# Performance work log

Measured on AMD Instinct MI355X. Metric: run time of the kernel, lower is better.

## Reference

```python
import jax, jax.numpy as jnp
import numpy as np

B, E, D = 4096, 64, 1024

def setup_inputs() -> dict:
    key = jax.random.key(0)
    k1, k2 = jax.random.split(key)
    z = jax.random.normal(k1, (B, D), dtype=jnp.float32)
    expert_keys = jax.random.normal(k2, (E, D), dtype=jnp.float32)
    log_sigma = jnp.zeros((D,), dtype=jnp.float32)
    return {"z": z, "expert_keys": expert_keys, "log_sigma": log_sigma}

def reference(z, expert_keys, log_sigma):
    # diag(sigma_inv) @ diff followed by (. * diff).sum(-1) is exactly an
    # elementwise-scaled squared distance: sum_d exp(-log_sigma_d) * diff_d^2
    sigma_inv = jnp.exp(-log_sigma)                              # [D]
    diff = z[:, None, :] - expert_keys[None, :, :]               # [B, E, D]
    mahalanobis_dist = jnp.einsum('bed,d,bed->be', diff, sigma_inv, diff)  # [B, E]
    similarity = 1.0 / (1.0 + mahalanobis_dist)                  # [B, E]
    weights = jax.nn.softmax(similarity, axis=-1)                # [B, E]
    weighted_expert = weights @ expert_keys                      # [B, D]
    return (similarity, weighted_expert)
```

## Files before the change

kernel.cpp:

```cpp
#include <hip/hip_runtime.h>
#include <hip/hip_bf16.h>

#define B_N 4096
#define E_N 64
#define D_N 1024

typedef __bf16 bf16x8 __attribute__((ext_vector_type(8)));
typedef __bf16 bf16x4 __attribute__((ext_vector_type(4)));
typedef float f32x4 __attribute__((ext_vector_type(4)));


__global__ __launch_bounds__(256) void prep_kernel(
    const float* __restrict__ keys, const float* __restrict__ lsig,
    float* __restrict__ sinv, float* __restrict__ ak,
    __bf16* __restrict__ sk, __bf16* __restrict__ kT)
{
  const int e = blockIdx.x;
  const int t = threadIdx.x;
  const float4 k4 = *(const float4*)(keys + e * D_N + 4 * t);
  const float4 l4 = *(const float4*)(lsig + 4 * t);
  float4 s4;
  s4.x = expf(-l4.x); s4.y = expf(-l4.y); s4.z = expf(-l4.z); s4.w = expf(-l4.w);
  if (e == 0) *(float4*)(sinv + 4 * t) = s4;
  const float4 sk4 = make_float4(s4.x * k4.x, s4.y * k4.y, s4.z * k4.z, s4.w * k4.w);
  bf16x4 skb;
  skb[0] = (__bf16)sk4.x; skb[1] = (__bf16)sk4.y; skb[2] = (__bf16)sk4.z; skb[3] = (__bf16)sk4.w;
  *(bf16x4*)(sk + e * D_N + 4 * t) = skb;
  kT[(4 * t + 0) * E_N + e] = (__bf16)k4.x;
  kT[(4 * t + 1) * E_N + e] = (__bf16)k4.y;
  kT[(4 * t + 2) * E_N + e] = (__bf16)k4.z;
  kT[(4 * t + 3) * E_N + e] = (__bf16)k4.w;
  float p = sk4.x * k4.x + sk4.y * k4.y + sk4.z * k4.z + sk4.w * k4.w;
  #pragma unroll
  for (int off = 32; off > 0; off >>= 1) p += __shfl_down(p, off);
  __shared__ float red[4];
  if ((t & 63) == 0) red[t >> 6] = p;
  __syncthreads();
  if (t == 0) ak[e] = red[0] + red[1] + red[2] + red[3];
}

__global__ __launch_bounds__(256) void main_kernel(
    const float* __restrict__ z, const float* __restrict__ sinv,
    const float* __restrict__ ak, const __bf16* __restrict__ sk,
    const __bf16* __restrict__ kT,
    float* __restrict__ out_sim, float* __restrict__ out_we)
{
  constexpr int ZS = D_N + 8;
  __shared__ __bf16 zlds[16 * ZS];
  __shared__ float azp[16][16];
  __shared__ float azs[16];
  __shared__ float simb[16][68];
  __shared__ __bf16 wlds[16][72];

  const int t  = threadIdx.x;
  const int b0 = blockIdx.x * 16;

  const int sr = t >> 4;
  const int sc = t & 15;
  const float* zrow = z + (size_t)(b0 + sr) * D_N;
  float azacc = 0.f;
  #pragma unroll
  for (int l = 0; l < 16; ++l) {
    const int c = sc * 4 + l * 64;
    const float4 z4 = *(const float4*)(zrow + c);
    const float4 s4 = *(const float4*)(sinv + c);
    azacc += s4.x * z4.x * z4.x; azacc += s4.y * z4.y * z4.y;
    azacc += s4.z * z4.z * z4.z; azacc += s4.w * z4.w * z4.w;
    bf16x4 zb;
    zb[0] = (__bf16)z4.x; zb[1] = (__bf16)z4.y; zb[2] = (__bf16)z4.z; zb[3] = (__bf16)z4.w;
    *(bf16x4*)(&zlds[sr * ZS + c]) = zb;
  }
  azp[sr][sc] = azacc;
  __syncthreads();
  if (t < 16) {
    float s = 0.f;
    #pragma unroll
    for (int i = 0; i < 16; ++i) s += azp[t][i];
    azs[t] = s;
  }

  const int wave = t >> 6;
  const int lane = t & 63;
  const int ln = lane & 15;
  const int q  = lane >> 4;

  f32x4 acc = {0.f, 0.f, 0.f, 0.f};
  const __bf16* bp = sk + (size_t)(wave * 16 + ln) * D_N + q * 8;
  const __bf16* ap = &zlds[ln * ZS + q * 8];
  #pragma unroll 8
  for (int ks = 0; ks < 32; ++ks) {
    const bf16x8 bfr = *(const bf16x8*)(bp + ks * 32);
    const bf16x8 afr = *(const bf16x8*)(ap + ks * 32);
    acc = __builtin_amdgcn_mfma_f32_16x16x32_bf16(afr, bfr, acc, 0, 0, 0);
  }

  const float akv = ak[wave * 16 + ln];
  __syncthreads();
  #pragma unroll
  for (int i = 0; i < 4; ++i) {
    const int row = q * 4 + i;
    const float dist = azs[row] + akv - 2.0f * acc[i];
    simb[row][wave * 16 + ln] = 1.0f / (1.0f + dist);
  }
  __syncthreads();

  if (t < 64) {
    const int row = t >> 2, seg = t & 3;
    float v[16];
    #pragma unroll
    for (int i = 0; i < 16; ++i) v[i] = simb[row][seg * 16 + i];
    float mx = v[0];
    #pragma unroll
    for (int i = 1; i < 16; ++i) mx = fmaxf(mx, v[i]);
    mx = fmaxf(mx, __shfl_xor(mx, 1));
    mx = fmaxf(mx, __shfl_xor(mx, 2));
    float sum = 0.f;
    #pragma unroll
    for (int i = 0; i < 16; ++i) { v[i] = __expf(v[i] - mx); sum += v[i]; }
    sum += __shfl_xor(sum, 1);
    sum += __shfl_xor(sum, 2);
    const float inv = 1.0f / sum;
    #pragma unroll
    for (int i = 0; i < 16; ++i) wlds[row][seg * 16 + i] = (__bf16)(v[i] * inv);
  }
  __syncthreads();

  {
    const float4 sv = *(const float4*)&simb[t >> 4][(t & 15) * 4];
    *(float4*)(out_sim + (size_t)(b0 + (t >> 4)) * E_N + (t & 15) * 4) = sv;
  }

  const bf16x8 a0 = *(const bf16x8*)&wlds[ln][q * 8];
  const bf16x8 a1 = *(const bf16x8*)&wlds[ln][32 + q * 8];
  #pragma unroll 4
  for (int i = 0; i < 16; ++i) {
    const int dt = wave + 4 * i;
    const int d0 = dt * 16;
    const __bf16* kp = kT + (size_t)(d0 + ln) * E_N + q * 8;
    const bf16x8 b0f = *(const bf16x8*)(kp);
    const bf16x8 b1f = *(const bf16x8*)(kp + 32);
    f32x4 o = {0.f, 0.f, 0.f, 0.f};
    o = __builtin_amdgcn_mfma_f32_16x16x32_bf16(a0, b0f, o, 0, 0, 0);
    o = __builtin_amdgcn_mfma_f32_16x16x32_bf16(a1, b1f, o, 0, 0, 0);
    #pragma unroll
    for (int j = 0; j < 4; ++j)
      out_we[(size_t)(b0 + q * 4 + j) * D_N + d0 + ln] = o[j];
  }
}

extern "C" void kernel_launch(void* const* d_in, const int* in_sizes, int n_in,
                              void* d_out, int out_size, void* d_ws, size_t ws_size,
                              hipStream_t stream)
{
  const float* z    = (const float*)d_in[0];
  const float* keys = (const float*)d_in[1];
  const float* ls   = (const float*)d_in[2];
  float* out_sim = (float*)d_out;
  float* out_we  = out_sim + (size_t)B_N * E_N;
  char* ws = (char*)d_ws;
  float*  sinv = (float*)(ws);
  float*  ak   = (float*)(ws + 4096);
  __bf16* sk   = (__bf16*)(ws + 4352);
  __bf16* kT   = (__bf16*)(ws + 135424);
  prep_kernel<<<E_N, 256, 0, stream>>>(keys, ls, sinv, ak, sk, kT);
  main_kernel<<<B_N / 16, 256, 0, stream>>>(z, sinv, ak, sk, kT, out_sim, out_we);
}
```

Measured before the change: 85.86 us.

## Halve rows per block, stage output through LDS, tile-transpose keys in prep

The main kernel now handles 8 batch rows per block instead of 16, which doubles the grid to 512 blocks for better CU occupancy. Half the MFMA rows are computed and then discarded. The weighted-expert output is staged per wave in LDS so it can be written as coalesced float4 rows instead of scattered scalar stores. The az reduction now uses wave shuffles instead of an LDS pass. The prep kernel gets 16 extra blocks that transpose the keys through LDS into kT with vectorized stores, replacing strided 2-byte global writes. In exchange, the redundant MFMA work and the extra LDS traffic add cost.

New measurement: 89.13 us. +3.8%, slower.

```diff
diff --git a/kernel.cpp b/kernel.cpp
--- a/kernel.cpp
+++ b/kernel.cpp
@@ -4,6 +4,7 @@
 #define B_N 4096
 #define E_N 64
 #define D_N 1024
+#define ROWS 8
 
 typedef __bf16 bf16x8 __attribute__((ext_vector_type(8)));
 typedef __bf16 bf16x4 __attribute__((ext_vector_type(4)));
@@ -15,28 +16,47 @@
     float* __restrict__ sinv, float* __restrict__ ak,
     __bf16* __restrict__ sk, __bf16* __restrict__ kT)
 {
-  const int e = blockIdx.x;
+  __shared__ float red[4];
+  __shared__ __bf16 tl[64][72];
+  const int bid = blockIdx.x;
   const int t = threadIdx.x;
-  const float4 k4 = *(const float4*)(keys + e * D_N + 4 * t);
-  const float4 l4 = *(const float4*)(lsig + 4 * t);
-  float4 s4;
-  s4.x = expf(-l4.x); s4.y = expf(-l4.y); s4.z = expf(-l4.z); s4.w = expf(-l4.w);
-  if (e == 0) *(float4*)(sinv + 4 * t) = s4;
-  const float4 sk4 = make_float4(s4.x * k4.x, s4.y * k4.y, s4.z * k4.z, s4.w * k4.w);
-  bf16x4 skb;
-  skb[0] = (__bf16)sk4.x; skb[1] = (__bf16)sk4.y; skb[2] = (__bf16)sk4.z; skb[3] = (__bf16)sk4.w;
-  *(bf16x4*)(sk + e * D_N + 4 * t) = skb;
-  kT[(4 * t + 0) * E_N + e] = (__bf16)k4.x;
-  kT[(4 * t + 1) * E_N + e] = (__bf16)k4.y;
-  kT[(4 * t + 2) * E_N + e] = (__bf16)k4.z;
-  kT[(4 * t + 3) * E_N + e] = (__bf16)k4.w;
-  float p = sk4.x * k4.x + sk4.y * k4.y + sk4.z * k4.z + sk4.w * k4.w;
-  #pragma unroll
-  for (int off = 32; off > 0; off >>= 1) p += __shfl_down(p, off);
-  __shared__ float red[4];
-  if ((t & 63) == 0) red[t >> 6] = p;
-  __syncthreads();
-  if (t == 0) ak[e] = red[0] + red[1] + red[2] + red[3];
+
+  if (bid < 64) {
+    const int e = bid;
+    const float4 k4 = *(const float4*)(keys + e * D_N + 4 * t);
+    const float4 l4 = *(const float4*)(lsig + 4 * t);
+    float4 s4;
+    s4.x = expf(-l4.x); s4.y = expf(-l4.y); s4.z = expf(-l4.z); s4.w = expf(-l4.w);
+    if (e == 0) *(float4*)(sinv + 4 * t) = s4;
+    const float4 sk4 = make_float4(s4.x * k4.x, s4.y * k4.y, s4.z * k4.z, s4.w * k4.w);
+    bf16x4 skb;
+    skb[0] = (__bf16)sk4.x; skb[1] = (__bf16)sk4.y; skb[2] = (__bf16)sk4.z; skb[3] = (__bf16)sk4.w;
+    *(bf16x4*)(sk + e * D_N + 4 * t) = skb;
+    float p = sk4.x * k4.x + sk4.y * k4.y + sk4.z * k4.z + sk4.w * k4.w;
+    #pragma unroll
+    for (int off = 32; off > 0; off >>= 1) p += __shfl_down(p, off);
+    if ((t & 63) == 0) red[t >> 6] = p;
+    __syncthreads();
+    if (t == 0) ak[e] = red[0] + red[1] + red[2] + red[3];
+  } else {
+    const int d0 = (bid - 64) * 64;
+    #pragma unroll
+    for (int p = 0; p < 4; ++p) {
+      const int e  = p * 16 + (t >> 4);
+      const int dd = (t & 15) * 4;
+      const float4 k4 = *(const float4*)(keys + (size_t)e * D_N + d0 + dd);
+      tl[dd + 0][e] = (__bf16)k4.x; tl[dd + 1][e] = (__bf16)k4.y;
+      tl[dd + 2][e] = (__bf16)k4.z; tl[dd + 3][e] = (__bf16)k4.w;
+    }
+    __syncthreads();
+    #pragma unroll
+    for (int p = 0; p < 2; ++p) {
+      const int dd = p * 32 + (t >> 3);
+      const int l8 = t & 7;
+      const bf16x8 v = *(const bf16x8*)&tl[dd][l8 * 8];
+      *(bf16x8*)(kT + (size_t)(d0 + dd) * E_N + l8 * 8) = v;
+    }
+  }
 }
 
 __global__ __launch_bounds__(256) void main_kernel(
@@ -46,38 +66,34 @@
     float* __restrict__ out_sim, float* __restrict__ out_we)
 {
   constexpr int ZS = D_N + 8;
-  __shared__ __bf16 zlds[16 * ZS];
-  __shared__ float azp[16][16];
-  __shared__ float azs[16];
-  __shared__ float simb[16][68];
-  __shared__ __bf16 wlds[16][72];
+  __shared__ __bf16 zlds[ROWS * ZS];
+  __shared__ float azs[ROWS];
+  __shared__ float simb[ROWS][68];
+  __shared__ __bf16 wlds[ROWS][72];
+  __shared__ float estage[4][ROWS][64];
 
   const int t  = threadIdx.x;
-  const int b0 = blockIdx.x * 16;
+  const int b0 = blockIdx.x * ROWS;
 
-  const int sr = t >> 4;
-  const int sc = t & 15;
+  const int sr = t >> 5;
+  const int sc = t & 31;
   const float* zrow = z + (size_t)(b0 + sr) * D_N;
-  float azacc = 0.f;
+  float az = 0.f;
   #pragma unroll
-  for (int l = 0; l < 16; ++l) {
-    const int c = sc * 4 + l * 64;
+  for (int l = 0; l < 8; ++l) {
+    const int c = sc * 4 + l * 128;
     const float4 z4 = *(const float4*)(zrow + c);
     const float4 s4 = *(const float4*)(sinv + c);
-    azacc += s4.x * z4.x * z4.x; azacc += s4.y * z4.y * z4.y;
-    azacc += s4.z * z4.z * z4.z; azacc += s4.w * z4.w * z4.w;
+    az += s4.x * z4.x * z4.x + s4.y * z4.y * z4.y + s4.z * z4.z * z4.z + s4.w * z4.w * z4.w;
     bf16x4 zb;
     zb[0] = (__bf16)z4.x; zb[1] = (__bf16)z4.y; zb[2] = (__bf16)z4.z; zb[3] = (__bf16)z4.w;
     *(bf16x4*)(&zlds[sr * ZS + c]) = zb;
   }
-  azp[sr][sc] = azacc;
+  az += __shfl_down(az, 16); az += __shfl_down(az, 8);
+  az += __shfl_down(az, 4);  az += __shfl_down(az, 2);
+  az += __shfl_down(az, 1);
+  if (sc == 0) azs[sr] = az;
   __syncthreads();
-  if (t < 16) {
-    float s = 0.f;
-    #pragma unroll
-    for (int i = 0; i < 16; ++i) s += azp[t][i];
-    azs[t] = s;
-  }
 
   const int wave = t >> 6;
   const int lane = t & 63;
@@ -86,25 +102,25 @@
 
   f32x4 acc = {0.f, 0.f, 0.f, 0.f};
   const __bf16* bp = sk + (size_t)(wave * 16 + ln) * D_N + q * 8;
-  const __bf16* ap = &zlds[ln * ZS + q * 8];
+  const __bf16* ap = &zlds[(ln & 7) * ZS + q * 8];
   #pragma unroll 8
   for (int ks = 0; ks < 32; ++ks) {
     const bf16x8 bfr = *(const bf16x8*)(bp + ks * 32);
     const bf16x8 afr = *(const bf16x8*)(ap + ks * 32);
     acc = __builtin_amdgcn_mfma_f32_16x16x32_bf16(afr, bfr, acc, 0, 0, 0);
   }
-
   const float akv = ak[wave * 16 + ln];
-  __syncthreads();
-  #pragma unroll
-  for (int i = 0; i < 4; ++i) {
-    const int row = q * 4 + i;
-    const float dist = azs[row] + akv - 2.0f * acc[i];
-    simb[row][wave * 16 + ln] = 1.0f / (1.0f + dist);
+  if (q < 2) {
+    #pragma unroll
+    for (int i = 0; i < 4; ++i) {
+      const int row = q * 4 + i;
+      const float dist = azs[row] + akv - 2.0f * acc[i];
+      simb[row][wave * 16 + ln] = 1.0f / (1.0f + dist);
+    }
   }
   __syncthreads();
 
-  if (t < 64) {
+  if (t < 32) {
     const int row = t >> 2, seg = t & 3;
     float v[16];
     #pragma unroll
@@ -125,26 +141,40 @@
   }
   __syncthreads();
 
-  {
+  if (t < 128) {
     const float4 sv = *(const float4*)&simb[t >> 4][(t & 15) * 4];
     *(float4*)(out_sim + (size_t)(b0 + (t >> 4)) * E_N + (t & 15) * 4) = sv;
   }
 
-  const bf16x8 a0 = *(const bf16x8*)&wlds[ln][q * 8];
-  const bf16x8 a1 = *(const bf16x8*)&wlds[ln][32 + q * 8];
-  #pragma unroll 4
-  for (int i = 0; i < 16; ++i) {
-    const int dt = wave + 4 * i;
-    const int d0 = dt * 16;
-    const __bf16* kp = kT + (size_t)(d0 + ln) * E_N + q * 8;
-    const bf16x8 b0f = *(const bf16x8*)(kp);
-    const bf16x8 b1f = *(const bf16x8*)(kp + 32);
-    f32x4 o = {0.f, 0.f, 0.f, 0.f};
-    o = __builtin_amdgcn_mfma_f32_16x16x32_bf16(a0, b0f, o, 0, 0, 0);
-    o = __builtin_amdgcn_mfma_f32_16x16x32_bf16(a1, b1f, o, 0, 0, 0);
+  const bf16x8 a0 = *(const bf16x8*)&wlds[ln & 7][q * 8];
+  const bf16x8 a1 = *(const bf16x8*)&wlds[ln & 7][32 + q * 8];
+  #pragma unroll
+  for (int g = 0; g < 4; ++g) {
     #pragma unroll
-    for (int j = 0; j < 4; ++j)
-      out_we[(size_t)(b0 + q * 4 + j) * D_N + d0 + ln] = o[j];
+    for (int i2 = 0; i2 < 4; ++i2) {
+      const int dt = wave * 16 + g * 4 + i2;
+      const int d0 = dt * 16;
+      const __bf16* kp = kT + (size_t)(d0 + ln) * E_N + q * 8;
+      const bf16x8 b0f = *(const bf16x8*)(kp);
+      const bf16x8 b1f = *(const bf16x8*)(kp + 32);
+      f32x4 o = {0.f, 0.f, 0.f, 0.f};
+      o = __builtin_amdgcn_mfma_f32_16x16x32_bf16(a0, b0f, o, 0, 0, 0);
+      o = __builtin_amdgcn_mfma_f32_16x16x32_bf16(a1, b1f, o, 0, 0, 0);
+      if (q < 2) {
+        #pragma unroll
+        for (int j = 0; j < 4; ++j)
+          estage[wave][q * 4 + j][i2 * 16 + ln] = o[j];
+      }
+    }
+    __builtin_amdgcn_wave_barrier();
+    #pragma unroll
+    for (int j2 = 0; j2 < 2; ++j2) {
+      const int f = j2 * 256 + lane * 4;
+      const int row = f >> 6, col = f & 63;
+      const float4 v = *(const float4*)&estage[wave][row][col];
+      *(float4*)(out_we + (size_t)(b0 + row) * D_N + wave * 256 + g * 64 + col) = v;
+    }
+    __builtin_amdgcn_wave_barrier();
   }
 }
 
@@ -162,6 +192,6 @@
   float*  ak   = (float*)(ws + 4096);
   __bf16* sk   = (__bf16*)(ws + 4352);
   __bf16* kT   = (__bf16*)(ws + 135424);
-  prep_kernel<<<E_N, 256, 0, stream>>>(keys, ls, sinv, ak, sk, kT);
-  main_kernel<<<B_N / 16, 256, 0, stream>>>(z, sinv, ak, sk, kT, out_sim, out_we);
+  prep_kernel<<<80, 256, 0, stream>>>(keys, ls, sinv, ak, sk, kT);
+  main_kernel<<<B_N / ROWS, 256, 0, stream>>>(z, sinv, ak, sk, kT, out_sim, out_we);
 }
```
